# Kernel optimization log

Measured on AMD Instinct MI355X. Metric: run time of the kernel, lower is better.

The kernel has to match this reference:

```python
import jax, jax.numpy as jnp
import numpy as np

N, E, C, H, L = 20000, 200000, 64, 4, 2
L0_IN, E_IN, L0_OUT = 65, 15, 64
HC = H * C
EPS = 1e-5  # InstanceNorm1d default eps
NEG_SLOPE = 0.01  # F.leaky_relu default used by DGL EGATConv


def setup_inputs() -> dict:
    key = jax.random.key(0)
    ks = jax.random.split(key, 16)
    def s(k, shape, fan):
        return (jax.random.normal(k, shape, jnp.float32) / np.float32(np.sqrt(fan)))
    return {
        "x": jax.random.normal(ks[0], (N, L0_IN), jnp.float32),
        "efeat": jax.random.normal(ks[1], (E, E_IN), jnp.float32),
        "src": jax.random.randint(ks[2], (E,), 0, N, dtype=jnp.int32),
        "dst": jax.random.randint(ks[3], (E,), 0, N, dtype=jnp.int32),
        "Wn0": s(ks[4], (L0_IN, C), L0_IN),
        "bn0": jnp.zeros((C,), jnp.float32),
        "We0": s(ks[5], (E_IN, C), E_IN),
        "be0": jnp.zeros((C,), jnp.float32),
        "Wnode": s(ks[6], (L, C, HC), C),
        "bnode": jnp.zeros((L, HC), jnp.float32),
        "Wni": s(ks[7], (L, C, HC), C),
        "Wnj": s(ks[8], (L, C, HC), C),
        "Wfij": s(ks[9], (L, C, HC), C),
        "attn": s(ks[10], (L, H, C), C),
        "bias_e": jnp.zeros((L, HC), jnp.float32),
        "Wf": s(ks[11], (C, L0_OUT), C),
        "bf": jnp.zeros((L0_OUT,), jnp.float32),
    }


def _inorm(x):
    # InstanceNorm1d on a 2D [rows, channels] tensor == per-row normalization
    m = jnp.mean(x, axis=-1, keepdims=True)
    v = jnp.var(x, axis=-1, keepdims=True)
    return (x - m) * jax.lax.rsqrt(v + EPS)


def reference(x, efeat, src, dst, Wn0, bn0, We0, be0, Wnode, bnode,
              Wni, Wnj, Wfij, attn, bias_e, Wf, bf):
    h = x @ Wn0 + bn0        # [N, C]
    f = efeat @ We0 + be0    # [E, C]
    for l in range(L):
        # edge feature update: f_out = fc_ni(h)[src] + fc_nj(h)[dst] + fc_fij(f) + bias
        f_out = (h @ Wni[l])[src] + (h @ Wnj[l])[dst] + f @ Wfij[l] + bias_e[l]  # [E, HC]
        e = jax.nn.leaky_relu(f_out, NEG_SLOPE).reshape(E, H, C)
        score = jnp.einsum('ehc,hc->eh', e, attn[l])  # [E, H]
        # edge softmax over incoming edges of each destination node
        smax = jax.ops.segment_max(score, dst, num_segments=N)
        w = jnp.exp(score - smax[dst])
        denom = jax.ops.segment_sum(w, dst, num_segments=N)
        a = w / denom[dst]                                # [E, H]
        hproj = (h @ Wnode[l] + bnode[l]).reshape(N, H, C)
        msg = hproj[src] * a[:, :, None]                  # [E, H, C]
        h_new = jax.ops.segment_sum(msg, dst, num_segments=N)  # [N, H, C]
        # mean over heads -> InstanceNorm -> ELU
        h = jax.nn.elu(_inorm(jnp.mean(h_new, axis=1)))
        f = jax.nn.elu(_inorm(jnp.mean(f_out.reshape(E, H, C), axis=1)))
    return h @ Wf + bf
```

## Files before the change

kernel.cpp:

```cpp
#include <hip/hip_runtime.h>
#include <cmath>

#define NN 20000
#define NE 200000
#define SCAN_BLOCKS 79

typedef __attribute__((ext_vector_type(8))) short bf16x8;
typedef __attribute__((ext_vector_type(4))) float f32x4;
typedef unsigned int uint;

__device__ __forceinline__ float4 ld4(const float* p){ return *(const float4*)p; }

__device__ __forceinline__ uint packbf(float a, float b) {
  uint ua = __float_as_uint(a);
  uint ub = __float_as_uint(b);
  ua = (ua + 0x7fffu + ((ua >> 16) & 1u)) >> 16;
  ub = (ub + 0x7fffu + ((ub >> 16) & 1u)) >> 16;
  return ua | (ub << 16);
}
__device__ __forceinline__ float4 up4(uint2 u) {
  return make_float4(__uint_as_float(u.x << 16), __uint_as_float(u.x & 0xffff0000u),
                     __uint_as_float(u.y << 16), __uint_as_float(u.y & 0xffff0000u));
}

__global__ void gemm4_bf16(const float* __restrict__ A, const float* __restrict__ B,
                           const float* __restrict__ bias, uint2* __restrict__ O,
                           int M, int K, int Nout) {
  int jt = Nout >> 2;
  int idx = blockIdx.x * 256 + threadIdx.x;
  if (idx >= M * jt) return;
  int m = idx / jt;
  int j4 = (idx - m * jt) << 2;
  const float* a = A + (long)m * K;
  const float* b = B + j4;
  float ax = 0.f, ay = 0.f, az = 0.f, aw = 0.f;
  for (int k = 0; k < K; k++) {
    float av = a[k];
    float4 bv = ld4(b + (long)k * Nout);
    ax = fmaf(av, bv.x, ax); ay = fmaf(av, bv.y, ay);
    az = fmaf(av, bv.z, az); aw = fmaf(av, bv.w, aw);
  }
  if (bias) { float4 bb = ld4(bias + j4); ax += bb.x; ay += bb.y; az += bb.z; aw += bb.w; }
  O[(long)m * jt + (j4 >> 2)] = make_uint2(packbf(ax, ay), packbf(az, aw));
}

__global__ void zero_i32(int* __restrict__ p, int n) {
  int i = blockIdx.x * 256 + threadIdx.x;
  if (i < n) p[i] = 0;
}

__global__ void count_deg(const int* __restrict__ dst, int* __restrict__ deg) {
  int e = blockIdx.x * 256 + threadIdx.x;
  if (e < NE) atomicAdd(&deg[dst[e]], 1);
}

__global__ void scan1(const int* __restrict__ deg, int* __restrict__ off, int* __restrict__ bsum) {
  __shared__ int buf[256];
  int t = threadIdx.x;
  int g = blockIdx.x * 256 + t;
  int v = (g < NN) ? deg[g] : 0;
  buf[t] = v;
  __syncthreads();
  for (int s = 1; s < 256; s <<= 1) {
    int x = (t >= s) ? buf[t - s] : 0;
    __syncthreads();
    buf[t] += x;
    __syncthreads();
  }
  if (g < NN) off[g] = buf[t] - v;
  if (t == 255) bsum[blockIdx.x] = buf[255];
}

__global__ void scan2(int* __restrict__ bsum, int* __restrict__ off) {
  __shared__ int buf[128];
  int t = threadIdx.x;
  int v = (t < SCAN_BLOCKS) ? bsum[t] : 0;
  buf[t] = v;
  __syncthreads();
  for (int s = 1; s < 128; s <<= 1) {
    int x = (t >= s) ? buf[t - s] : 0;
    __syncthreads();
    buf[t] += x;
    __syncthreads();
  }
  if (t < SCAN_BLOCKS) bsum[t] = buf[t] - v;
  if (t == 127) off[NN] = buf[127];
}

__global__ void scan3(int* __restrict__ off, const int* __restrict__ bsum) {
  int g = blockIdx.x * 256 + threadIdx.x;
  if (g < NN) off[g] += bsum[blockIdx.x];
}

__global__ void fill_csr(const int* __restrict__ dst, const int* __restrict__ src,
                         const int* __restrict__ off, int* __restrict__ cursor,
                         int* __restrict__ esrc, int* __restrict__ csr_pos) {
  int e = blockIdx.x * 256 + threadIdx.x;
  if (e >= NE) return;
  int d = dst[e];
  int p = atomicAdd(&cursor[d], 1);
  int pos = off[d] + p;
  esrc[pos] = src[e];
  csr_pos[e] = pos;
}

__global__ void prep_w(const float* __restrict__ Wni, const float* __restrict__ Wnj,
                       const float* __restrict__ Wfij, const float* __restrict__ Wnode,
                       const float* __restrict__ bnode,
                       uint* __restrict__ Wcat, uint* __restrict__ WcT,
                       float* __restrict__ bmean) {
  int rid = blockIdx.x * 256 + threadIdx.x;
  if (rid < 512) {
    int l = rid >> 8, c = rid & 255;
    uint* D = Wcat + (size_t)l * 24576 + c * 96;
    for (int k8 = 0; k8 < 24; k8++) {
      int ss = k8 >> 3;
      const float* S = (ss == 0 ? Wni : ss == 1 ? Wnj : Wfij) + l * 16384;
      int kl = (k8 & 7) * 8;
      uint u0 = packbf(S[(kl+0)*256 + c], S[(kl+1)*256 + c]);
      uint u1 = packbf(S[(kl+2)*256 + c], S[(kl+3)*256 + c]);
      uint u2 = packbf(S[(kl+4)*256 + c], S[(kl+5)*256 + c]);
      uint u3 = packbf(S[(kl+6)*256 + c], S[(kl+7)*256 + c]);
      *((uint4*)(D + k8 * 4)) = make_uint4(u0, u1, u2, u3);
    }
  } else if (rid < 640) {
    int idx = rid - 512;
    int l = idx >> 6, c = idx & 63;
    const float* S = Wnode + l * 16384;
    uint* D = WcT + (size_t)l * 8192 + c * 128;
    for (int kp = 0; kp < 128; kp++) {
      int k0 = kp * 2, k1 = kp * 2 + 1;
      float v0 = S[(k0 & 63) * 256 + (k0 >> 6) * 64 + c] * 0.25f;
      float v1 = S[(k1 & 63) * 256 + (k1 >> 6) * 64 + c] * 0.25f;
      D[kp] = packbf(v0, v1);
    }
  } else if (rid < 768) {
    int idx = rid - 640;
    int l = idx >> 6, c = idx & 63;
    const float* S = bnode + l * 256;
    bmean[l * 64 + c] = 0.25f * (S[c] + S[64 + c] + S[128 + c] + S[192 + c]);
  }
}

__global__ __launch_bounds__(256) void edge_mfma(
    const uint4* __restrict__ f_bf, const uint4* __restrict__ h_bf,
    const uint* __restrict__ Wcat_l, const float* __restrict__ be_l,
    const float* __restrict__ attn_l, const int* __restrict__ src,
    const int* __restrict__ dst, float* __restrict__ sc_part,
    uint2* __restrict__ f_mid)
{
  int t = threadIdx.x, lane = t & 63, w = t >> 6;
  int col = lane & 15, quad = lane >> 4;
  bf16x8 A[4][6];
  float4 be4[4], at4[4];
  #pragma unroll
  for (int hg = 0; hg < 4; hg++) {
    int c = (4 * hg + w) * 16 + col;
    #pragma unroll
    for (int kt = 0; kt < 6; kt++)
      A[hg][kt] = *(const bf16x8*)&Wcat_l[c * 96 + kt * 16 + quad * 4];
    int ce = (4 * hg + w) * 16 + quad * 4;
    be4[hg] = ld4(be_l + ce);
    at4[hg] = ld4(attn_l + ce);
  }
  #pragma unroll 1
  for (int ch = 0; ch < 4; ch++) {
    int e = blockIdx.x * 64 + ch * 16 + col;
    int s_ = src[e], d_ = dst[e];
    bf16x8 B[6];
    B[0] = *(const bf16x8*)&h_bf[(long)s_ * 8 + quad];
    B[1] = *(const bf16x8*)&h_bf[(long)s_ * 8 + 4 + quad];
    B[2] = *(const bf16x8*)&h_bf[(long)d_ * 8 + quad];
    B[3] = *(const bf16x8*)&h_bf[(long)d_ * 8 + 4 + quad];
    B[4] = *(const bf16x8*)&f_bf[(long)e * 8 + quad];
    B[5] = *(const bf16x8*)&f_bf[(long)e * 8 + 4 + quad];
    float m0 = 0.f, m1 = 0.f, m2 = 0.f, m3 = 0.f;
    float sh0 = 0.f, sh1 = 0.f, sh2 = 0.f, sh3 = 0.f;
    #pragma unroll
    for (int hg = 0; hg < 4; hg++) {
      f32x4 acc = (f32x4){0.f, 0.f, 0.f, 0.f};
      #pragma unroll
      for (int kt = 0; kt < 6; kt++)
        acc = __builtin_amdgcn_mfma_f32_16x16x32_bf16(A[hg][kt], B[kt], acc, 0, 0, 0);
      float x0 = acc[0] + be4[hg].x;
      float x1 = acc[1] + be4[hg].y;
      float x2 = acc[2] + be4[hg].z;
      float x3 = acc[3] + be4[hg].w;
      float l0 = x0 > 0.f ? x0 : 0.01f * x0;
      float l1 = x1 > 0.f ? x1 : 0.01f * x1;
      float l2 = x2 > 0.f ? x2 : 0.01f * x2;
      float l3 = x3 > 0.f ? x3 : 0.01f * x3;
      float dp = l0 * at4[hg].x + l1 * at4[hg].y + l2 * at4[hg].z + l3 * at4[hg].w;
      if (hg == 0) sh0 = dp; else if (hg == 1) sh1 = dp;
      else if (hg == 2) sh2 = dp; else sh3 = dp;
      m0 += x0; m1 += x1; m2 += x2; m3 += x3;
    }
    m0 *= 0.25f; m1 *= 0.25f; m2 *= 0.25f; m3 *= 0.25f;
    sh0 += __shfl_xor(sh0, 16); sh0 += __shfl_xor(sh0, 32);
    sh1 += __shfl_xor(sh1, 16); sh1 += __shfl_xor(sh1, 32);
    sh2 += __shfl_xor(sh2, 16); sh2 += __shfl_xor(sh2, 32);
    sh3 += __shfl_xor(sh3, 16); sh3 += __shfl_xor(sh3, 32);
    if (quad == 0)
      *(float4*)&sc_part[(long)e * 16 + w * 4] = make_float4(sh0, sh1, sh2, sh3);
    f_mid[(long)e * 16 + w * 4 + quad] = make_uint2(packbf(m0, m1), packbf(m2, m3));
  }
}

__global__ __launch_bounds__(256) void fixup(
    const uint4* __restrict__ f_mid4, const float4* __restrict__ sc_part4,
    const int* __restrict__ csr_pos, uint4* __restrict__ f_next4,
    float4* __restrict__ sc_csr4)
{
  int tid = blockIdx.x * 256 + threadIdx.x;
  int e = tid >> 3, sub = tid & 7;
  uint4 mv = f_mid4[(long)e * 8 + sub];
  float4 p0 = up4(make_uint2(mv.x, mv.y));
  float4 p1 = up4(make_uint2(mv.z, mv.w));
  float s1 = p0.x + p0.y + p0.z + p0.w + p1.x + p1.y + p1.z + p1.w;
  float s2 = p0.x*p0.x + p0.y*p0.y + p0.z*p0.z + p0.w*p0.w
           + p1.x*p1.x + p1.y*p1.y + p1.z*p1.z + p1.w*p1.w;
  s1 += __shfl_xor(s1, 1); s2 += __shfl_xor(s2, 1);
  s1 += __shfl_xor(s1, 2); s2 += __shfl_xor(s2, 2);
  s1 += __shfl_xor(s1, 4); s2 += __shfl_xor(s2, 4);
  float mean = s1 * 0.015625f;
  float var  = s2 * 0.015625f - mean * mean;
  float rs = rsqrtf(var + 1e-5f);
  float o0 = (p0.x - mean) * rs; o0 = o0 > 0.f ? o0 : expm1f(o0);
  float o1 = (p0.y - mean) * rs; o1 = o1 > 0.f ? o1 : expm1f(o1);
  float o2 = (p0.z - mean) * rs; o2 = o2 > 0.f ? o2 : expm1f(o2);
  float o3 = (p0.w - mean) * rs; o3 = o3 > 0.f ? o3 : expm1f(o3);
  float o4 = (p1.x - mean) * rs; o4 = o4 > 0.f ? o4 : expm1f(o4);
  float o5 = (p1.y - mean) * rs; o5 = o5 > 0.f ? o5 : expm1f(o5);
  float o6 = (p1.z - mean) * rs; o6 = o6 > 0.f ? o6 : expm1f(o6);
  float o7 = (p1.w - mean) * rs; o7 = o7 > 0.f ? o7 : expm1f(o7);
  f_next4[(long)e * 8 + sub] =
      make_uint4(packbf(o0, o1), packbf(o2, o3), packbf(o4, o5), packbf(o6, o7));
  if (sub < 4) {
    float4 sp = sc_part4[(long)e * 4 + sub];
    sp.x += __shfl_xor(sp.x, 1); sp.y += __shfl_xor(sp.y, 1);
    sp.z += __shfl_xor(sp.z, 1); sp.w += __shfl_xor(sp.w, 1);
    sp.x += __shfl_xor(sp.x, 2); sp.y += __shfl_xor(sp.y, 2);
    sp.z += __shfl_xor(sp.z, 2); sp.w += __shfl_xor(sp.w, 2);
    if (sub == 0) sc_csr4[csr_pos[e]] = sp;
  }
}

__global__ __launch_bounds__(256) void agg_kernel(
    const uint* __restrict__ h_u, const float4* __restrict__ sc_csr4,
    const int* __restrict__ esrc, const int* __restrict__ off,
    uint* __restrict__ g_u)
{
  int n = (blockIdx.x * 256 + threadIdx.x) >> 6;
  int lane = threadIdx.x & 63;
  int half = lane >> 5, seg = lane & 31;
  int o0 = off[n], o1 = off[n + 1];
  if (o0 == o1) {
    g_u[(long)n * 128 + (half * 2) * 32 + seg] = 0u;
    g_u[(long)n * 128 + (half * 2 + 1) * 32 + seg] = 0u;
    return;
  }
  float mx0 = -3.0e38f, mx1 = -3.0e38f, mx2 = -3.0e38f, mx3 = -3.0e38f;
  for (int i = o0 + half; i < o1; i += 2) {
    float4 s = sc_csr4[i];
    mx0 = fmaxf(mx0, s.x); mx1 = fmaxf(mx1, s.y);
    mx2 = fmaxf(mx2, s.z); mx3 = fmaxf(mx3, s.w);
  }
  mx0 = fmaxf(mx0, __shfl_xor(mx0, 32)); mx1 = fmaxf(mx1, __shfl_xor(mx1, 32));
  mx2 = fmaxf(mx2, __shfl_xor(mx2, 32)); mx3 = fmaxf(mx3, __shfl_xor(mx3, 32));
  float d0 = 0.f, d1 = 0.f, d2 = 0.f, d3 = 0.f;
  float a00=0.f,a01=0.f,a10=0.f,a11=0.f,a20=0.f,a21=0.f,a30=0.f,a31=0.f;
  for (int i = o0 + half; i < o1; i += 2) {
    float4 s = sc_csr4[i];
    float w0 = __expf(s.x - mx0), w1 = __expf(s.y - mx1);
    float w2 = __expf(s.z - mx2), w3 = __expf(s.w - mx3);
    d0 += w0; d1 += w1; d2 += w2; d3 += w3;
    int sr = esrc[i];
    uint hv = h_u[(long)sr * 32 + seg];
    float hlo = __uint_as_float(hv << 16);
    float hhi = __uint_as_float(hv & 0xffff0000u);
    a00 = fmaf(w0, hlo, a00); a01 = fmaf(w0, hhi, a01);
    a10 = fmaf(w1, hlo, a10); a11 = fmaf(w1, hhi, a11);
    a20 = fmaf(w2, hlo, a20); a21 = fmaf(w2, hhi, a21);
    a30 = fmaf(w3, hlo, a30); a31 = fmaf(w3, hhi, a31);
  }
  d0 += __shfl_xor(d0, 32); d1 += __shfl_xor(d1, 32);
  d2 += __shfl_xor(d2, 32); d3 += __shfl_xor(d3, 32);
  a00 += __shfl_xor(a00, 32); a01 += __shfl_xor(a01, 32);
  a10 += __shfl_xor(a10, 32); a11 += __shfl_xor(a11, 32);
  a20 += __shfl_xor(a20, 32); a21 += __shfl_xor(a21, 32);
  a30 += __shfl_xor(a30, 32); a31 += __shfl_xor(a31, 32);
  float i0 = 1.f / d0, i1 = 1.f / d1, i2 = 1.f / d2, i3 = 1.f / d3;
  uint u0 = packbf(a00 * i0, a01 * i0);
  uint u1 = packbf(a10 * i1, a11 * i1);
  uint u2 = packbf(a20 * i2, a21 * i2);
  uint u3 = packbf(a30 * i3, a31 * i3);
  if (half == 0) {
    g_u[(long)n * 128 + seg] = u0;
    g_u[(long)n * 128 + 32 + seg] = u1;
  } else {
    g_u[(long)n * 128 + 64 + seg] = u2;
    g_u[(long)n * 128 + 96 + seg] = u3;
  }
}

__global__ __launch_bounds__(256) void combine(
    const uint4* __restrict__ g4, const uint4* __restrict__ WcT4,
    const float* __restrict__ bmean_l, const int* __restrict__ off,
    uint2* __restrict__ h_next)
{
  __shared__ float red[2][4][16][2];
  int t = threadIdx.x, lane = t & 63, w = t >> 6;
  int col = lane & 15, quad = lane >> 4;
  int c = w * 16 + col;
  bf16x8 A[8];
  #pragma unroll
  for (int kt = 0; kt < 8; kt++)
    A[kt] = *(const bf16x8*)&WcT4[c * 32 + kt * 4 + quad];
  int c2 = w * 16 + quad * 4;
  float4 bm = ld4(bmean_l + c2);
  for (int ch = 0; ch < 2; ch++) {
    int n = blockIdx.x * 32 + ch * 16 + col;
    int deg = off[n + 1] - off[n];
    f32x4 acc = (f32x4){0.f, 0.f, 0.f, 0.f};
    #pragma unroll
    for (int kt = 0; kt < 8; kt++) {
      bf16x8 B = *(const bf16x8*)&g4[(long)n * 32 + kt * 4 + quad];
      acc = __builtin_amdgcn_mfma_f32_16x16x32_bf16(A[kt], B, acc, 0, 0, 0);
    }
    float x0, x1, x2, x3;
    if (deg > 0) { x0 = acc[0] + bm.x; x1 = acc[1] + bm.y; x2 = acc[2] + bm.z; x3 = acc[3] + bm.w; }
    else { x0 = x1 = x2 = x3 = 0.f; }
    float s1 = x0 + x1 + x2 + x3;
    float s2 = x0*x0 + x1*x1 + x2*x2 + x3*x3;
    s1 += __shfl_xor(s1, 16); s2 += __shfl_xor(s2, 16);
    s1 += __shfl_xor(s1, 32); s2 += __shfl_xor(s2, 32);
    if (quad == 0) { red[ch][w][col][0] = s1; red[ch][w][col][1] = s2; }
    __syncthreads();
    float s1T = red[ch][0][col][0] + red[ch][1][col][0] + red[ch][2][col][0] + red[ch][3][col][0];
    float s2T = red[ch][0][col][1] + red[ch][1][col][1] + red[ch][2][col][1] + red[ch][3][col][1];
    float mean = s1T * 0.015625f;
    float var  = s2T * 0.015625f - mean * mean;
    float rs = rsqrtf(var + 1e-5f);
    float o0 = (x0 - mean) * rs; o0 = o0 > 0.f ? o0 : expm1f(o0);
    float o1 = (x1 - mean) * rs; o1 = o1 > 0.f ? o1 : expm1f(o1);
    float o2 = (x2 - mean) * rs; o2 = o2 > 0.f ? o2 : expm1f(o2);
    float o3 = (x3 - mean) * rs; o3 = o3 > 0.f ? o3 : expm1f(o3);
    h_next[(long)n * 16 + w * 4 + quad] = make_uint2(packbf(o0, o1), packbf(o2, o3));
  }
}

__global__ void final_gemm(const uint2* __restrict__ h, const float* __restrict__ Wf,
                           const float* __restrict__ bf_, float* __restrict__ out) {
  int idx = blockIdx.x * 256 + threadIdx.x;
  if (idx >= NN * 16) return;
  int m = idx >> 4, j4 = (idx & 15) << 2;
  const uint2* row = h + (long)m * 16;
  float ax = 0.f, ay = 0.f, az = 0.f, aw = 0.f;
  for (int kk = 0; kk < 16; kk++) {
    float4 a = up4(row[kk]);
    float4 b0 = ld4(Wf + (kk * 4 + 0) * 64 + j4);
    float4 b1 = ld4(Wf + (kk * 4 + 1) * 64 + j4);
    float4 b2 = ld4(Wf + (kk * 4 + 2) * 64 + j4);
    float4 b3 = ld4(Wf + (kk * 4 + 3) * 64 + j4);
    ax = fmaf(a.x, b0.x, ax); ay = fmaf(a.x, b0.y, ay); az = fmaf(a.x, b0.z, az); aw = fmaf(a.x, b0.w, aw);
    ax = fmaf(a.y, b1.x, ax); ay = fmaf(a.y, b1.y, ay); az = fmaf(a.y, b1.z, az); aw = fmaf(a.y, b1.w, aw);
    ax = fmaf(a.z, b2.x, ax); ay = fmaf(a.z, b2.y, ay); az = fmaf(a.z, b2.z, az); aw = fmaf(a.z, b2.w, aw);
    ax = fmaf(a.w, b3.x, ax); ay = fmaf(a.w, b3.y, ay); az = fmaf(a.w, b3.z, az); aw = fmaf(a.w, b3.w, aw);
  }
  float4 bb = ld4(bf_ + j4);
  *(float4*)(out + (long)m * 64 + j4) = make_float4(ax + bb.x, ay + bb.y, az + bb.z, aw + bb.w);
}

extern "C" void kernel_launch(void* const* d_in, const int* in_sizes, int n_in,
                              void* d_out, int out_size, void* d_ws, size_t ws_size,
                              hipStream_t stream) {
  const float* x      = (const float*)d_in[0];
  const float* efeat  = (const float*)d_in[1];
  const int*   src    = (const int*)d_in[2];
  const int*   dst    = (const int*)d_in[3];
  const float* Wn0    = (const float*)d_in[4];
  const float* bn0    = (const float*)d_in[5];
  const float* We0    = (const float*)d_in[6];
  const float* be0    = (const float*)d_in[7];
  const float* Wnode  = (const float*)d_in[8];
  const float* bnode  = (const float*)d_in[9];
  const float* Wni    = (const float*)d_in[10];
  const float* Wnj    = (const float*)d_in[11];
  const float* Wfij   = (const float*)d_in[12];
  const float* attn   = (const float*)d_in[13];
  const float* bias_e = (const float*)d_in[14];
  const float* Wf     = (const float*)d_in[15];
  const float* bf     = (const float*)d_in[16];
  float* out = (float*)d_out;

  char* w = (char*)d_ws;
  auto alloc = [&](size_t nbytes) { char* p = w; w += (nbytes + 255) & ~(size_t)255; return p; };
  uint2* h_a   = (uint2*)alloc((size_t)NN * 128);
  uint2* h_b   = (uint2*)alloc((size_t)NN * 128);
  uint2* f_a   = (uint2*)alloc((size_t)NE * 128);
  uint2* f_b   = (uint2*)alloc((size_t)NE * 128);
  uint2* f_mid = (uint2*)alloc((size_t)NE * 128);
  float* scp   = (float*)alloc((size_t)NE * 64);
  float* scc   = (float*)alloc((size_t)NE * 16);
  uint*  g     = (uint*)alloc((size_t)NN * 512);
  uint*  Wcat  = (uint*)alloc((size_t)2 * 24576 * 4);
  uint*  WcT   = (uint*)alloc((size_t)2 * 8192 * 4);
  float* bmean = (float*)alloc((size_t)2 * 64 * 4);
  int* deg     = (int*)alloc((size_t)NN * 2 * 4);
  int* cursor  = deg + NN;
  int* off     = (int*)alloc((size_t)(NN + 1) * 4);
  int* esrc    = (int*)alloc((size_t)NE * 4);
  int* csr_pos = (int*)alloc((size_t)NE * 4);
  int* bsum    = (int*)alloc((size_t)128 * 4);

  gemm4_bf16<<<(NN * 16 + 255) / 256, 256, 0, stream>>>(x, Wn0, bn0, h_a, NN, 65, 64);
  gemm4_bf16<<<(NE * 16 + 255) / 256, 256, 0, stream>>>(efeat, We0, be0, f_a, NE, 15, 64);
  prep_w<<<4, 256, 0, stream>>>(Wni, Wnj, Wfij, Wnode, bnode, Wcat, WcT, bmean);

  zero_i32<<<(2 * NN + 255) / 256, 256, 0, stream>>>(deg, 2 * NN);
  count_deg<<<(NE + 255) / 256, 256, 0, stream>>>(dst, deg);
  scan1<<<SCAN_BLOCKS, 256, 0, stream>>>(deg, off, bsum);
  scan2<<<1, 128, 0, stream>>>(bsum, off);
  scan3<<<SCAN_BLOCKS, 256, 0, stream>>>(off, bsum);
  fill_csr<<<(NE + 255) / 256, 256, 0, stream>>>(dst, src, off, cursor, esrc, csr_pos);

  uint2* hc = h_a; uint2* hn = h_b;
  uint2* fc = f_a; uint2* fn = f_b;
  for (int l = 0; l < 2; l++) {
    const uint* Wcat_l = Wcat + (size_t)l * 24576;
    const uint4* WcT_l = (const uint4*)(WcT + (size_t)l * 8192);
    const float* bm_l  = bmean + (size_t)l * 64;
    const float* be_l  = bias_e + (size_t)l * 256;
    const float* at_l  = attn + (size_t)l * 256;
    edge_mfma<<<NE / 64, 256, 0, stream>>>((const uint4*)fc, (const uint4*)hc,
                                           Wcat_l, be_l, at_l, src, dst, scp, f_mid);
    fixup<<<NE / 32, 256, 0, stream>>>((const uint4*)f_mid, (const float4*)scp,
                                       csr_pos, (uint4*)fn, (float4*)scc);
    agg_kernel<<<NN / 4, 256, 0, stream>>>((const uint*)hc, (const float4*)scc,
                                           esrc, off, g);
    combine<<<NN / 32, 256, 0, stream>>>((const uint4*)g, WcT_l, bm_l, off, hn);
    uint2* tmp = hc; hc = hn; hn = tmp;
    tmp = fc; fc = fn; fn = tmp;
  }
  final_gemm<<<(NN * 16 + 255) / 256, 256, 0, stream>>>(hc, Wf, bf, out);
}
```

Baseline: 500.2 us.

## Fuse edge fixup into edge MFMA kernel and aggregation with combine

Moves the per-edge instance norm, ELU and score reduction into the edge MFMA kernel through a shared-memory cross-wave reduction, which removes the f_mid and score-partial intermediates and the fixup launch. Fuses softmax aggregation with the node projection MFMA by staging the aggregated rows in LDS, which removes the g buffer round trip. The edge kernel now handles two 16-edge tiles per MFMA pass and streams weights from memory instead of holding them in registers. The initial GEMM also computes 16 outputs per thread. The tradeoffs are higher register and LDS pressure and extra block barriers.

```diff
diff --git a/kernel.cpp b/kernel.cpp
--- a/kernel.cpp
+++ b/kernel.cpp
@@ -23,25 +23,32 @@
                      __uint_as_float(u.y << 16), __uint_as_float(u.y & 0xffff0000u));
 }
 
-__global__ void gemm4_bf16(const float* __restrict__ A, const float* __restrict__ B,
-                           const float* __restrict__ bias, uint2* __restrict__ O,
-                           int M, int K, int Nout) {
-  int jt = Nout >> 2;
+__global__ void gemm16_bf16(const float* __restrict__ A, const float* __restrict__ B,
+                            const float* __restrict__ bias, uint2* __restrict__ O,
+                            int M, int K) {
   int idx = blockIdx.x * 256 + threadIdx.x;
-  if (idx >= M * jt) return;
-  int m = idx / jt;
-  int j4 = (idx - m * jt) << 2;
+  if (idx >= M * 4) return;
+  int m = idx >> 2, jq = idx & 3;
   const float* a = A + (long)m * K;
-  const float* b = B + j4;
-  float ax = 0.f, ay = 0.f, az = 0.f, aw = 0.f;
+  const float* b = B + jq * 16;
+  float c00=0,c01=0,c02=0,c03=0,c04=0,c05=0,c06=0,c07=0;
+  float c08=0,c09=0,c10=0,c11=0,c12=0,c13=0,c14=0,c15=0;
   for (int k = 0; k < K; k++) {
     float av = a[k];
-    float4 bv = ld4(b + (long)k * Nout);
-    ax = fmaf(av, bv.x, ax); ay = fmaf(av, bv.y, ay);
-    az = fmaf(av, bv.z, az); aw = fmaf(av, bv.w, aw);
-  }
-  if (bias) { float4 bb = ld4(bias + j4); ax += bb.x; ay += bb.y; az += bb.z; aw += bb.w; }
-  O[(long)m * jt + (j4 >> 2)] = make_uint2(packbf(ax, ay), packbf(az, aw));
+    const float* br = b + (long)k * 64;
+    float4 b0 = ld4(br), b1 = ld4(br + 4), b2 = ld4(br + 8), b3 = ld4(br + 12);
+    c00 = fmaf(av, b0.x, c00); c01 = fmaf(av, b0.y, c01); c02 = fmaf(av, b0.z, c02); c03 = fmaf(av, b0.w, c03);
+    c04 = fmaf(av, b1.x, c04); c05 = fmaf(av, b1.y, c05); c06 = fmaf(av, b1.z, c06); c07 = fmaf(av, b1.w, c07);
+    c08 = fmaf(av, b2.x, c08); c09 = fmaf(av, b2.y, c09); c10 = fmaf(av, b2.z, c10); c11 = fmaf(av, b2.w, c11);
+    c12 = fmaf(av, b3.x, c12); c13 = fmaf(av, b3.y, c13); c14 = fmaf(av, b3.z, c14); c15 = fmaf(av, b3.w, c15);
+  }
+  const float* bb = bias + jq * 16;
+  float4 v0 = ld4(bb), v1 = ld4(bb + 4), v2 = ld4(bb + 8), v3 = ld4(bb + 12);
+  uint2* op = O + (long)m * 16 + jq * 4;
+  op[0] = make_uint2(packbf(c00 + v0.x, c01 + v0.y), packbf(c02 + v0.z, c03 + v0.w));
+  op[1] = make_uint2(packbf(c04 + v1.x, c05 + v1.y), packbf(c06 + v1.z, c07 + v1.w));
+  op[2] = make_uint2(packbf(c08 + v2.x, c09 + v2.y), packbf(c10 + v2.z, c11 + v2.w));
+  op[3] = make_uint2(packbf(c12 + v3.x, c13 + v3.y), packbf(c14 + v3.z, c15 + v3.w));
 }
 
 __global__ void zero_i32(int* __restrict__ p, int n) {
@@ -146,207 +153,224 @@
     const uint4* __restrict__ f_bf, const uint4* __restrict__ h_bf,
     const uint* __restrict__ Wcat_l, const float* __restrict__ be_l,
     const float* __restrict__ attn_l, const int* __restrict__ src,
-    const int* __restrict__ dst, float* __restrict__ sc_part,
-    uint2* __restrict__ f_mid)
+    const int* __restrict__ dst, const int* __restrict__ csr_pos,
+    float* __restrict__ scc, uint2* __restrict__ f_next)
 {
+  __shared__ float red[4][2][33][6];
   int t = threadIdx.x, lane = t & 63, w = t >> 6;
   int col = lane & 15, quad = lane >> 4;
-  bf16x8 A[4][6];
   float4 be4[4], at4[4];
   #pragma unroll
   for (int hg = 0; hg < 4; hg++) {
-    int c = (4 * hg + w) * 16 + col;
-    #pragma unroll
-    for (int kt = 0; kt < 6; kt++)
-      A[hg][kt] = *(const bf16x8*)&Wcat_l[c * 96 + kt * 16 + quad * 4];
     int ce = (4 * hg + w) * 16 + quad * 4;
     be4[hg] = ld4(be_l + ce);
     at4[hg] = ld4(attn_l + ce);
   }
+  float ma[2][2][4];
   #pragma unroll 1
-  for (int ch = 0; ch < 4; ch++) {
-    int e = blockIdx.x * 64 + ch * 16 + col;
-    int s_ = src[e], d_ = dst[e];
-    bf16x8 B[6];
-    B[0] = *(const bf16x8*)&h_bf[(long)s_ * 8 + quad];
-    B[1] = *(const bf16x8*)&h_bf[(long)s_ * 8 + 4 + quad];
-    B[2] = *(const bf16x8*)&h_bf[(long)d_ * 8 + quad];
-    B[3] = *(const bf16x8*)&h_bf[(long)d_ * 8 + 4 + quad];
-    B[4] = *(const bf16x8*)&f_bf[(long)e * 8 + quad];
-    B[5] = *(const bf16x8*)&f_bf[(long)e * 8 + 4 + quad];
-    float m0 = 0.f, m1 = 0.f, m2 = 0.f, m3 = 0.f;
-    float sh0 = 0.f, sh1 = 0.f, sh2 = 0.f, sh3 = 0.f;
+  for (int ch = 0; ch < 2; ch++) {
+    int ea = blockIdx.x * 64 + ch * 32 + col;
+    int eb = ea + 16;
+    int sa = src[ea], da = dst[ea];
+    int sb = src[eb], db = dst[eb];
+    bf16x8 Ba[6], Bb[6];
+    Ba[0] = *(const bf16x8*)&h_bf[(long)sa * 8 + quad];
+    Ba[1] = *(const bf16x8*)&h_bf[(long)sa * 8 + 4 + quad];
+    Ba[2] = *(const bf16x8*)&h_bf[(long)da * 8 + quad];
+    Ba[3] = *(const bf16x8*)&h_bf[(long)da * 8 + 4 + quad];
+    Ba[4] = *(const bf16x8*)&f_bf[(long)ea * 8 + quad];
+    Ba[5] = *(const bf16x8*)&f_bf[(long)ea * 8 + 4 + quad];
+    Bb[0] = *(const bf16x8*)&h_bf[(long)sb * 8 + quad];
+    Bb[1] = *(const bf16x8*)&h_bf[(long)sb * 8 + 4 + quad];
+    Bb[2] = *(const bf16x8*)&h_bf[(long)db * 8 + quad];
+    Bb[3] = *(const bf16x8*)&h_bf[(long)db * 8 + 4 + quad];
+    Bb[4] = *(const bf16x8*)&f_bf[(long)eb * 8 + quad];
+    Bb[5] = *(const bf16x8*)&f_bf[(long)eb * 8 + 4 + quad];
+    float ma0 = 0.f, ma1 = 0.f, ma2 = 0.f, ma3 = 0.f;
+    float mb0 = 0.f, mb1 = 0.f, mb2 = 0.f, mb3 = 0.f;
+    float sa0 = 0.f, sa1 = 0.f, sa2 = 0.f, sa3 = 0.f;
+    float sb0 = 0.f, sb1 = 0.f, sb2 = 0.f, sb3 = 0.f;
     #pragma unroll
     for (int hg = 0; hg < 4; hg++) {
-      f32x4 acc = (f32x4){0.f, 0.f, 0.f, 0.f};
+      f32x4 aa = (f32x4){0.f, 0.f, 0.f, 0.f};
+      f32x4 ab = (f32x4){0.f, 0.f, 0.f, 0.f};
+      const uint* Ab = &Wcat_l[((4 * hg + w) * 16 + col) * 96 + quad * 4];
       #pragma unroll
-      for (int kt = 0; kt < 6; kt++)
-        acc = __builtin_amdgcn_mfma_f32_16x16x32_bf16(A[hg][kt], B[kt], acc, 0, 0, 0);
-      float x0 = acc[0] + be4[hg].x;
-      float x1 = acc[1] + be4[hg].y;
-      float x2 = acc[2] + be4[hg].z;
-      float x3 = acc[3] + be4[hg].w;
-      float l0 = x0 > 0.f ? x0 : 0.01f * x0;
-      float l1 = x1 > 0.f ? x1 : 0.01f * x1;
-      float l2 = x2 > 0.f ? x2 : 0.01f * x2;
-      float l3 = x3 > 0.f ? x3 : 0.01f * x3;
-      float dp = l0 * at4[hg].x + l1 * at4[hg].y + l2 * at4[hg].z + l3 * at4[hg].w;
-      if (hg == 0) sh0 = dp; else if (hg == 1) sh1 = dp;
-      else if (hg == 2) sh2 = dp; else sh3 = dp;
-      m0 += x0; m1 += x1; m2 += x2; m3 += x3;
-    }
-    m0 *= 0.25f; m1 *= 0.25f; m2 *= 0.25f; m3 *= 0.25f;
-    sh0 += __shfl_xor(sh0, 16); sh0 += __shfl_xor(sh0, 32);
-    sh1 += __shfl_xor(sh1, 16); sh1 += __shfl_xor(sh1, 32);
-    sh2 += __shfl_xor(sh2, 16); sh2 += __shfl_xor(sh2, 32);
-    sh3 += __shfl_xor(sh3, 16); sh3 += __shfl_xor(sh3, 32);
-    if (quad == 0)
-      *(float4*)&sc_part[(long)e * 16 + w * 4] = make_float4(sh0, sh1, sh2, sh3);
-    f_mid[(long)e * 16 + w * 4 + quad] = make_uint2(packbf(m0, m1), packbf(m2, m3));
-  }
-}
-
-__global__ __launch_bounds__(256) void fixup(
-    const uint4* __restrict__ f_mid4, const float4* __restrict__ sc_part4,
-    const int* __restrict__ csr_pos, uint4* __restrict__ f_next4,
-    float4* __restrict__ sc_csr4)
-{
-  int tid = blockIdx.x * 256 + threadIdx.x;
-  int e = tid >> 3, sub = tid & 7;
-  uint4 mv = f_mid4[(long)e * 8 + sub];
-  float4 p0 = up4(make_uint2(mv.x, mv.y));
-  float4 p1 = up4(make_uint2(mv.z, mv.w));
-  float s1 = p0.x + p0.y + p0.z + p0.w + p1.x + p1.y + p1.z + p1.w;
-  float s2 = p0.x*p0.x + p0.y*p0.y + p0.z*p0.z + p0.w*p0.w
-           + p1.x*p1.x + p1.y*p1.y + p1.z*p1.z + p1.w*p1.w;
-  s1 += __shfl_xor(s1, 1); s2 += __shfl_xor(s2, 1);
-  s1 += __shfl_xor(s1, 2); s2 += __shfl_xor(s2, 2);
-  s1 += __shfl_xor(s1, 4); s2 += __shfl_xor(s2, 4);
-  float mean = s1 * 0.015625f;
-  float var  = s2 * 0.015625f - mean * mean;
-  float rs = rsqrtf(var + 1e-5f);
-  float o0 = (p0.x - mean) * rs; o0 = o0 > 0.f ? o0 : expm1f(o0);
-  float o1 = (p0.y - mean) * rs; o1 = o1 > 0.f ? o1 : expm1f(o1);
-  float o2 = (p0.z - mean) * rs; o2 = o2 > 0.f ? o2 : expm1f(o2);
-  float o3 = (p0.w - mean) * rs; o3 = o3 > 0.f ? o3 : expm1f(o3);
-  float o4 = (p1.x - mean) * rs; o4 = o4 > 0.f ? o4 : expm1f(o4);
-  float o5 = (p1.y - mean) * rs; o5 = o5 > 0.f ? o5 : expm1f(o5);
-  float o6 = (p1.z - mean) * rs; o6 = o6 > 0.f ? o6 : expm1f(o6);
-  float o7 = (p1.w - mean) * rs; o7 = o7 > 0.f ? o7 : expm1f(o7);
-  f_next4[(long)e * 8 + sub] =
-      make_uint4(packbf(o0, o1), packbf(o2, o3), packbf(o4, o5), packbf(o6, o7));
-  if (sub < 4) {
-    float4 sp = sc_part4[(long)e * 4 + sub];
-    sp.x += __shfl_xor(sp.x, 1); sp.y += __shfl_xor(sp.y, 1);
-    sp.z += __shfl_xor(sp.z, 1); sp.w += __shfl_xor(sp.w, 1);
-    sp.x += __shfl_xor(sp.x, 2); sp.y += __shfl_xor(sp.y, 2);
-    sp.z += __shfl_xor(sp.z, 2); sp.w += __shfl_xor(sp.w, 2);
-    if (sub == 0) sc_csr4[csr_pos[e]] = sp;
-  }
-}
-
-__global__ __launch_bounds__(256) void agg_kernel(
+      for (int kt = 0; kt < 6; kt++) {
+        bf16x8 Af = *(const bf16x8*)(Ab + kt * 16);
+        aa = __builtin_amdgcn_mfma_f32_16x16x32_bf16(Af, Ba[kt], aa, 0, 0, 0);
+        ab = __builtin_amdgcn_mfma_f32_16x16x32_bf16(Af, Bb[kt], ab, 0, 0, 0);
+      }
+      float xa0 = aa[0] + be4[hg].x, xa1 = aa[1] + be4[hg].y;
+      float xa2 = aa[2] + be4[hg].z, xa3 = aa[3] + be4[hg].w;
+      float xb0 = ab[0] + be4[hg].x, xb1 = ab[1] + be4[hg].y;
+      float xb2 = ab[2] + be4[hg].z, xb3 = ab[3] + be4[hg].w;
+      float la0 = xa0 > 0.f ? xa0 : 0.01f * xa0;
+      float la1 = xa1 > 0.f ? xa1 : 0.01f * xa1;
+      float la2 = xa2 > 0.f ? xa2 : 0.01f * xa2;
+      float la3 = xa3 > 0.f ? xa3 : 0.01f * xa3;
+      float lb0 = xb0 > 0.f ? xb0 : 0.01f * xb0;
+      float lb1 = xb1 > 0.f ? xb1 : 0.01f * xb1;
+      float lb2 = xb2 > 0.f ? xb2 : 0.01f * xb2;
+      float lb3 = xb3 > 0.f ? xb3 : 0.01f * xb3;
+      float dpa = la0 * at4[hg].x + la1 * at4[hg].y + la2 * at4[hg].z + la3 * at4[hg].w;
+      float dpb = lb0 * at4[hg].x + lb1 * at4[hg].y + lb2 * at4[hg].z + lb3 * at4[hg].w;
+      if (hg == 0) { sa0 = dpa; sb0 = dpb; }
+      else if (hg == 1) { sa1 = dpa; sb1 = dpb; }
+      else if (hg == 2) { sa2 = dpa; sb2 = dpb; }
+      else { sa3 = dpa; sb3 = dpb; }
+      ma0 += xa0; ma1 += xa1; ma2 += xa2; ma3 += xa3;
+      mb0 += xb0; mb1 += xb1; mb2 += xb2; mb3 += xb3;
+    }
+    ma0 *= 0.25f; ma1 *= 0.25f; ma2 *= 0.25f; ma3 *= 0.25f;
+    mb0 *= 0.25f; mb1 *= 0.25f; mb2 *= 0.25f; mb3 *= 0.25f;
+    ma[ch][0][0] = ma0; ma[ch][0][1] = ma1; ma[ch][0][2] = ma2; ma[ch][0][3] = ma3;
+    ma[ch][1][0] = mb0; ma[ch][1][1] = mb1; ma[ch][1][2] = mb2; ma[ch][1][3] = mb3;
+    float s1a = ma0 + ma1 + ma2 + ma3;
+    float s2a = ma0*ma0 + ma1*ma1 + ma2*ma2 + ma3*ma3;
+    float s1b = mb0 + mb1 + mb2 + mb3;
+    float s2b = mb0*mb0 + mb1*mb1 + mb2*mb2 + mb3*mb3;
+    sa0 += __shfl_xor(sa0, 16); sa0 += __shfl_xor(sa0, 32);
+    sa1 += __shfl_xor(sa1, 16); sa1 += __shfl_xor(sa1, 32);
+    sa2 += __shfl_xor(sa2, 16); sa2 += __shfl_xor(sa2, 32);
+    sa3 += __shfl_xor(sa3, 16); sa3 += __shfl_xor(sa3, 32);
+    sb0 += __shfl_xor(sb0, 16); sb0 += __shfl_xor(sb0, 32);
+    sb1 += __shfl_xor(sb1, 16); sb1 += __shfl_xor(sb1, 32);
+    sb2 += __shfl_xor(sb2, 16); sb2 += __shfl_xor(sb2, 32);
+    sb3 += __shfl_xor(sb3, 16); sb3 += __shfl_xor(sb3, 32);
+    s1a += __shfl_xor(s1a, 16); s1a += __shfl_xor(s1a, 32);
+    s2a += __shfl_xor(s2a, 16); s2a += __shfl_xor(s2a, 32);
+    s1b += __shfl_xor(s1b, 16); s1b += __shfl_xor(s1b, 32);
+    s2b += __shfl_xor(s2b, 16); s2b += __shfl_xor(s2b, 32);
+    if (quad == 0) {
+      float* ra = &red[w][ch][col][0];
+      ra[0] = sa0; ra[1] = sa1; ra[2] = sa2; ra[3] = sa3; ra[4] = s1a; ra[5] = s2a;
+      float* rb = &red[w][ch][16 + col][0];
+      rb[0] = sb0; rb[1] = sb1; rb[2] = sb2; rb[3] = sb3; rb[4] = s1b; rb[5] = s2b;
+    }
+  }
+  __syncthreads();
+  {
+    int eL = t >> 2, hh = t & 3;
+    int e = blockIdx.x * 64 + eL;
+    int chx = eL >> 5, c32 = eL & 31;
+    float sv = red[0][chx][c32][hh] + red[1][chx][c32][hh]
+             + red[2][chx][c32][hh] + red[3][chx][c32][hh];
+    scc[(long)csr_pos[e] * 4 + hh] = sv;
+  }
+  #pragma unroll
+  for (int ch = 0; ch < 2; ch++) {
+    #pragma unroll
+    for (int sub = 0; sub < 2; sub++) {
+      int c32 = sub * 16 + col;
+      int e = blockIdx.x * 64 + ch * 32 + c32;
+      float s1T = red[0][ch][c32][4] + red[1][ch][c32][4]
+                + red[2][ch][c32][4] + red[3][ch][c32][4];
+      float s2T = red[0][ch][c32][5] + red[1][ch][c32][5]
+                + red[2][ch][c32][5] + red[3][ch][c32][5];
+      float mean = s1T * 0.015625f;
+      float var  = s2T * 0.015625f - mean * mean;
+      float rs = rsqrtf(var + 1e-5f);
+      float o0 = (ma[ch][sub][0] - mean) * rs; o0 = o0 > 0.f ? o0 : expm1f(o0);
+      float o1 = (ma[ch][sub][1] - mean) * rs; o1 = o1 > 0.f ? o1 : expm1f(o1);
+      float o2 = (ma[ch][sub][2] - mean) * rs; o2 = o2 > 0.f ? o2 : expm1f(o2);
+      float o3 = (ma[ch][sub][3] - mean) * rs; o3 = o3 > 0.f ? o3 : expm1f(o3);
+      f_next[(long)e * 16 + w * 4 + quad] = make_uint2(packbf(o0, o1), packbf(o2, o3));
+    }
+  }
+}
+
+__global__ __launch_bounds__(256) void agg_combine(
     const uint* __restrict__ h_u, const float4* __restrict__ sc_csr4,
     const int* __restrict__ esrc, const int* __restrict__ off,
-    uint* __restrict__ g_u)
-{
-  int n = (blockIdx.x * 256 + threadIdx.x) >> 6;
-  int lane = threadIdx.x & 63;
-  int half = lane >> 5, seg = lane & 31;
-  int o0 = off[n], o1 = off[n + 1];
-  if (o0 == o1) {
-    g_u[(long)n * 128 + (half * 2) * 32 + seg] = 0u;
-    g_u[(long)n * 128 + (half * 2 + 1) * 32 + seg] = 0u;
-    return;
-  }
-  float mx0 = -3.0e38f, mx1 = -3.0e38f, mx2 = -3.0e38f, mx3 = -3.0e38f;
-  for (int i = o0 + half; i < o1; i += 2) {
-    float4 s = sc_csr4[i];
-    mx0 = fmaxf(mx0, s.x); mx1 = fmaxf(mx1, s.y);
-    mx2 = fmaxf(mx2, s.z); mx3 = fmaxf(mx3, s.w);
-  }
-  mx0 = fmaxf(mx0, __shfl_xor(mx0, 32)); mx1 = fmaxf(mx1, __shfl_xor(mx1, 32));
-  mx2 = fmaxf(mx2, __shfl_xor(mx2, 32)); mx3 = fmaxf(mx3, __shfl_xor(mx3, 32));
-  float d0 = 0.f, d1 = 0.f, d2 = 0.f, d3 = 0.f;
-  float a00=0.f,a01=0.f,a10=0.f,a11=0.f,a20=0.f,a21=0.f,a30=0.f,a31=0.f;
-  for (int i = o0 + half; i < o1; i += 2) {
-    float4 s = sc_csr4[i];
-    float w0 = __expf(s.x - mx0), w1 = __expf(s.y - mx1);
-    float w2 = __expf(s.z - mx2), w3 = __expf(s.w - mx3);
-    d0 += w0; d1 += w1; d2 += w2; d3 += w3;
-    int sr = esrc[i];
-    uint hv = h_u[(long)sr * 32 + seg];
-    float hlo = __uint_as_float(hv << 16);
-    float hhi = __uint_as_float(hv & 0xffff0000u);
-    a00 = fmaf(w0, hlo, a00); a01 = fmaf(w0, hhi, a01);
-    a10 = fmaf(w1, hlo, a10); a11 = fmaf(w1, hhi, a11);
-    a20 = fmaf(w2, hlo, a20); a21 = fmaf(w2, hhi, a21);
-    a30 = fmaf(w3, hlo, a30); a31 = fmaf(w3, hhi, a31);
-  }
-  d0 += __shfl_xor(d0, 32); d1 += __shfl_xor(d1, 32);
-  d2 += __shfl_xor(d2, 32); d3 += __shfl_xor(d3, 32);
-  a00 += __shfl_xor(a00, 32); a01 += __shfl_xor(a01, 32);
-  a10 += __shfl_xor(a10, 32); a11 += __shfl_xor(a11, 32);
-  a20 += __shfl_xor(a20, 32); a21 += __shfl_xor(a21, 32);
-  a30 += __shfl_xor(a30, 32); a31 += __shfl_xor(a31, 32);
-  float i0 = 1.f / d0, i1 = 1.f / d1, i2 = 1.f / d2, i3 = 1.f / d3;
-  uint u0 = packbf(a00 * i0, a01 * i0);
-  uint u1 = packbf(a10 * i1, a11 * i1);
-  uint u2 = packbf(a20 * i2, a21 * i2);
-  uint u3 = packbf(a30 * i3, a31 * i3);
-  if (half == 0) {
-    g_u[(long)n * 128 + seg] = u0;
-    g_u[(long)n * 128 + 32 + seg] = u1;
-  } else {
-    g_u[(long)n * 128 + 64 + seg] = u2;
-    g_u[(long)n * 128 + 96 + seg] = u3;
-  }
-}
-
-__global__ __launch_bounds__(256) void combine(
-    const uint4* __restrict__ g4, const uint4* __restrict__ WcT4,
-    const float* __restrict__ bmean_l, const int* __restrict__ off,
+    const uint4* __restrict__ WcT4, const float* __restrict__ bmean_l,
     uint2* __restrict__ h_next)
 {
-  __shared__ float red[2][4][16][2];
+  __shared__ uint gsh[16][132];
+  __shared__ float red2[4][17][2];
   int t = threadIdx.x, lane = t & 63, w = t >> 6;
   int col = lane & 15, quad = lane >> 4;
-  int c = w * 16 + col;
-  bf16x8 A[8];
+  int half = lane >> 5, seg = lane & 31;
+  int n0 = blockIdx.x * 16;
+  bf16x8 A2[8];
   #pragma unroll
   for (int kt = 0; kt < 8; kt++)
-    A[kt] = *(const bf16x8*)&WcT4[c * 32 + kt * 4 + quad];
-  int c2 = w * 16 + quad * 4;
-  float4 bm = ld4(bmean_l + c2);
-  for (int ch = 0; ch < 2; ch++) {
-    int n = blockIdx.x * 32 + ch * 16 + col;
-    int deg = off[n + 1] - off[n];
-    f32x4 acc = (f32x4){0.f, 0.f, 0.f, 0.f};
-    #pragma unroll
-    for (int kt = 0; kt < 8; kt++) {
-      bf16x8 B = *(const bf16x8*)&g4[(long)n * 32 + kt * 4 + quad];
-      acc = __builtin_amdgcn_mfma_f32_16x16x32_bf16(A[kt], B, acc, 0, 0, 0);
-    }
-    float x0, x1, x2, x3;
-    if (deg > 0) { x0 = acc[0] + bm.x; x1 = acc[1] + bm.y; x2 = acc[2] + bm.z; x3 = acc[3] + bm.w; }
-    else { x0 = x1 = x2 = x3 = 0.f; }
-    float s1 = x0 + x1 + x2 + x3;
-    float s2 = x0*x0 + x1*x1 + x2*x2 + x3*x3;
-    s1 += __shfl_xor(s1, 16); s2 += __shfl_xor(s2, 16);
-    s1 += __shfl_xor(s1, 32); s2 += __shfl_xor(s2, 32);
-    if (quad == 0) { red[ch][w][col][0] = s1; red[ch][w][col][1] = s2; }
-    __syncthreads();
-    float s1T = red[ch][0][col][0] + red[ch][1][col][0] + red[ch][2][col][0] + red[ch][3][col][0];
-    float s2T = red[ch][0][col][1] + red[ch][1][col][1] + red[ch][2][col][1] + red[ch][3][col][1];
-    float mean = s1T * 0.015625f;
-    float var  = s2T * 0.015625f - mean * mean;
-    float rs = rsqrtf(var + 1e-5f);
-    float o0 = (x0 - mean) * rs; o0 = o0 > 0.f ? o0 : expm1f(o0);
-    float o1 = (x1 - mean) * rs; o1 = o1 > 0.f ? o1 : expm1f(o1);
-    float o2 = (x2 - mean) * rs; o2 = o2 > 0.f ? o2 : expm1f(o2);
-    float o3 = (x3 - mean) * rs; o3 = o3 > 0.f ? o3 : expm1f(o3);
-    h_next[(long)n * 16 + w * 4 + quad] = make_uint2(packbf(o0, o1), packbf(o2, o3));
-  }
+    A2[kt] = *(const bf16x8*)&WcT4[(w * 16 + col) * 32 + kt * 4 + quad];
+  #pragma unroll 1
+  for (int nl = 0; nl < 4; nl++) {
+    int n = n0 + w * 4 + nl;
+    int o0 = off[n], o1 = off[n + 1];
+    uint u0 = 0u, u1 = 0u, u2 = 0u, u3 = 0u;
+    if (o0 < o1) {
+      float mx0 = -3.0e38f, mx1 = -3.0e38f, mx2 = -3.0e38f, mx3 = -3.0e38f;
+      for (int i = o0 + half; i < o1; i += 2) {
+        float4 s = sc_csr4[i];
+        mx0 = fmaxf(mx0, s.x); mx1 = fmaxf(mx1, s.y);
+        mx2 = fmaxf(mx2, s.z); mx3 = fmaxf(mx3, s.w);
+      }
+      mx0 = fmaxf(mx0, __shfl_xor(mx0, 32)); mx1 = fmaxf(mx1, __shfl_xor(mx1, 32));
+      mx2 = fmaxf(mx2, __shfl_xor(mx2, 32)); mx3 = fmaxf(mx3, __shfl_xor(mx3, 32));
+      float d0 = 0.f, d1 = 0.f, d2 = 0.f, d3 = 0.f;
+      float a00=0.f,a01=0.f,a10=0.f,a11=0.f,a20=0.f,a21=0.f,a30=0.f,a31=0.f;
+      for (int i = o0 + half; i < o1; i += 2) {
+        float4 s = sc_csr4[i];
+        float w0 = __expf(s.x - mx0), w1 = __expf(s.y - mx1);
+        float w2 = __expf(s.z - mx2), w3 = __expf(s.w - mx3);
+        d0 += w0; d1 += w1; d2 += w2; d3 += w3;
+        int sr = esrc[i];
+        uint hv = h_u[(long)sr * 32 + seg];
+        float hlo = __uint_as_float(hv << 16);
+        float hhi = __uint_as_float(hv & 0xffff0000u);
+        a00 = fmaf(w0, hlo, a00); a01 = fmaf(w0, hhi, a01);
+        a10 = fmaf(w1, hlo, a10); a11 = fmaf(w1, hhi, a11);
+        a20 = fmaf(w2, hlo, a20); a21 = fmaf(w2, hhi, a21);
+        a30 = fmaf(w3, hlo, a30); a31 = fmaf(w3, hhi, a31);
+      }
+      d0 += __shfl_xor(d0, 32); d1 += __shfl_xor(d1, 32);
+      d2 += __shfl_xor(d2, 32); d3 += __shfl_xor(d3, 32);
+      a00 += __shfl_xor(a00, 32); a01 += __shfl_xor(a01, 32);
+      a10 += __shfl_xor(a10, 32); a11 += __shfl_xor(a11, 32);
+      a20 += __shfl_xor(a20, 32); a21 += __shfl_xor(a21, 32);
+      a30 += __shfl_xor(a30, 32); a31 += __shfl_xor(a31, 32);
+      float i0 = 1.f / d0, i1 = 1.f / d1, i2 = 1.f / d2, i3 = 1.f / d3;
+      u0 = packbf(a00 * i0, a01 * i0);
+      u1 = packbf(a10 * i1, a11 * i1);
+      u2 = packbf(a20 * i2, a21 * i2);
+      u3 = packbf(a30 * i3, a31 * i3);
+    }
+    int nloc = w * 4 + nl;
+    if (half == 0) { gsh[nloc][seg] = u0; gsh[nloc][32 + seg] = u1; }
+    else           { gsh[nloc][64 + seg] = u2; gsh[nloc][96 + seg] = u3; }
+  }
+  __syncthreads();
+  f32x4 acc = (f32x4){0.f, 0.f, 0.f, 0.f};
+  #pragma unroll
+  for (int kt = 0; kt < 8; kt++) {
+    bf16x8 Bg = *(const bf16x8*)&gsh[col][kt * 16 + quad * 4];
+    acc = __builtin_amdgcn_mfma_f32_16x16x32_bf16(A2[kt], Bg, acc, 0, 0, 0);
+  }
+  int n2 = n0 + col;
+  int dg = off[n2 + 1] - off[n2];
+  float4 bm = ld4(bmean_l + w * 16 + quad * 4);
+  float x0, x1, x2, x3;
+  if (dg > 0) { x0 = acc[0] + bm.x; x1 = acc[1] + bm.y; x2 = acc[2] + bm.z; x3 = acc[3] + bm.w; }
+  else { x0 = x1 = x2 = x3 = 0.f; }
+  float s1 = x0 + x1 + x2 + x3;
+  float s2 = x0*x0 + x1*x1 + x2*x2 + x3*x3;
+  s1 += __shfl_xor(s1, 16); s2 += __shfl_xor(s2, 16);
+  s1 += __shfl_xor(s1, 32); s2 += __shfl_xor(s2, 32);
+  if (quad == 0) { red2[w][col][0] = s1; red2[w][col][1] = s2; }
+  __syncthreads();
+  float s1T = red2[0][col][0] + red2[1][col][0] + red2[2][col][0] + red2[3][col][0];
+  float s2T = red2[0][col][1] + red2[1][col][1] + red2[2][col][1] + red2[3][col][1];
+  float mean = s1T * 0.015625f;
+  float var  = s2T * 0.015625f - mean * mean;
+  float rs = rsqrtf(var + 1e-5f);
+  float o0 = (x0 - mean) * rs; o0 = o0 > 0.f ? o0 : expm1f(o0);
+  float o1 = (x1 - mean) * rs; o1 = o1 > 0.f ? o1 : expm1f(o1);
+  float o2 = (x2 - mean) * rs; o2 = o2 > 0.f ? o2 : expm1f(o2);
+  float o3 = (x3 - mean) * rs; o3 = o3 > 0.f ? o3 : expm1f(o3);
+  h_next[(long)n2 * 16 + w * 4 + quad] = make_uint2(packbf(o0, o1), packbf(o2, o3));
 }
 
 __global__ void final_gemm(const uint2* __restrict__ h, const float* __restrict__ Wf,
@@ -399,10 +423,7 @@
   uint2* h_b   = (uint2*)alloc((size_t)NN * 128);
   uint2* f_a   = (uint2*)alloc((size_t)NE * 128);
   uint2* f_b   = (uint2*)alloc((size_t)NE * 128);
-  uint2* f_mid = (uint2*)alloc((size_t)NE * 128);
-  float* scp   = (float*)alloc((size_t)NE * 64);
   float* scc   = (float*)alloc((size_t)NE * 16);
-  uint*  g     = (uint*)alloc((size_t)NN * 512);
   uint*  Wcat  = (uint*)alloc((size_t)2 * 24576 * 4);
   uint*  WcT   = (uint*)alloc((size_t)2 * 8192 * 4);
   float* bmean = (float*)alloc((size_t)2 * 64 * 4);
@@ -413,8 +434,8 @@
   int* csr_pos = (int*)alloc((size_t)NE * 4);
   int* bsum    = (int*)alloc((size_t)128 * 4);
 
-  gemm4_bf16<<<(NN * 16 + 255) / 256, 256, 0, stream>>>(x, Wn0, bn0, h_a, NN, 65, 64);
-  gemm4_bf16<<<(NE * 16 + 255) / 256, 256, 0, stream>>>(efeat, We0, be0, f_a, NE, 15, 64);
+  gemm16_bf16<<<(NN * 4 + 255) / 256, 256, 0, stream>>>(x, Wn0, bn0, h_a, NN, 65);
+  gemm16_bf16<<<(NE * 4 + 255) / 256, 256, 0, stream>>>(efeat, We0, be0, f_a, NE, 15);
   prep_w<<<4, 256, 0, stream>>>(Wni, Wnj, Wfij, Wnode, bnode, Wcat, WcT, bmean);
 
   zero_i32<<<(2 * NN + 255) / 256, 256, 0, stream>>>(deg, 2 * NN);
@@ -433,12 +454,10 @@
     const float* be_l  = bias_e + (size_t)l * 256;
     const float* at_l  = attn + (size_t)l * 256;
     edge_mfma<<<NE / 64, 256, 0, stream>>>((const uint4*)fc, (const uint4*)hc,
-                                           Wcat_l, be_l, at_l, src, dst, scp, f_mid);
-    fixup<<<NE / 32, 256, 0, stream>>>((const uint4*)f_mid, (const float4*)scp,
-                                       csr_pos, (uint4*)fn, (float4*)scc);
-    agg_kernel<<<NN / 4, 256, 0, stream>>>((const uint*)hc, (const float4*)scc,
-                                           esrc, off, g);
-    combine<<<NN / 32, 256, 0, stream>>>((const uint4*)g, WcT_l, bm_l, off, hn);
+                                           Wcat_l, be_l, at_l, src, dst,
+                                           csr_pos, scc, fn);
+    agg_combine<<<NN / 16, 256, 0, stream>>>((const uint*)hc, (const float4*)scc,
+                                             esrc, off, WcT_l, bm_l, hn);
     uint2* tmp = hc; hc = hn; hn = tmp;
     tmp = fc; fc = fn; fn = tmp;
   }
```

Result: slower. 530.8 us (+6.1%).
